# Optimization experiments

Hardware: AMD Instinct MI355X
Metric: run time of the kernel (lower is better)

The kernel has to match this reference:

```python
import jax, jax.numpy as jnp
import numpy as np
from jax import lax

B, C, H, W = 16, 3, 256, 256
K = 3          # lbp kernel size (odd)
POOL = 3       # avg pool size (odd so shapes are preserved)
Q = 8          # quant_len


def _build_lbp_kernel():
    mid = K // 2
    idx_pairs = [((0, 0), (K - 1, K - 1)), ((0, mid), (K - 1, mid)),
                 ((0, K - 1), (K - 1, 0)), ((mid, K - 1), (mid, 0))]
    ks = []
    for a, b in idx_pairs:
        for pos in (a, b):
            k = np.zeros((C, K, K), np.float32)
            k[:, mid, mid] = 1.0
            k[:, pos[0], pos[1]] = -1.0
            ks.append(k)
    return jnp.asarray(np.stack(ks))  # [8, C, K, K]

LBP_KERNEL = _build_lbp_kernel()
# cartesian_prod(arange(Q), arange(Q)) -> first coord slowest (row-major)
IDXS = jnp.asarray(np.stack(np.meshgrid(np.arange(Q), np.arange(Q), indexing='ij'), -1)
                   .reshape(Q * Q, 2).astype(np.float32))  # [64, 2]


def _forward(x, w_expand, b_expand, w_conv, b_conv, w_final, b_final, clamp_low, clamp_high):
    b = x.shape[0]
    # avg_pool2d(kernel=POOL, stride=1, pad=POOL//2, count_include_pad=True)
    p = POOL // 2
    xp = jnp.pad(x, ((0, 0), (0, 0), (p, p), (p, p)))
    x = lax.reduce_window(xp, 0.0, lax.add, (1, 1, POOL, POOL), (1, 1, 1, 1), 'VALID') / (POOL * POOL)
    # 8-channel LBP difference conv, 'same' padding
    x = lax.conv_general_dilated(x, LBP_KERNEL, (1, 1), ((K // 2, K // 2), (K // 2, K // 2)),
                                 dimension_numbers=('NCHW', 'OIHW', 'NCHW'))  # [B,8,H,W]
    x = jnp.clip(x, clamp_low[0], clamp_high[0])
    b4 = b * 4
    v = x.reshape(b4, 2, H * W)                    # pairwise channels
    mn = v.min(-1)                                 # [b4,2]
    mx = v.max(-1)
    lev = mn[..., None] + (mx - mn)[..., None] * (jnp.arange(Q, dtype=v.dtype) / Q)  # [b4,2,Q]
    hi = jnp.concatenate([lev[..., 1:], mx[..., None]], -1)                          # [b4,2,Q]
    vq = v[:, :, None, :]                                                            # [b4,2,1,HW]
    # keep value if lev[l] <= v <= hi[l], else 0 (values equal to a boundary land in both bins)
    masked = jnp.where((vq >= lev[..., None]) & (vq <= hi[..., None]), vq, 0.0)      # [b4,2,Q,HW]
    # joint weighted histogram: sum_p v0[p in bin i] * v1[p in bin j]
    hist = jnp.einsum('bip,bjp->bij', masked[:, 0], masked[:, 1])                    # [b4,Q,Q]
    hist = (hist / jnp.sum(hist)).reshape(b4, Q * Q)
    feats = jnp.concatenate([jnp.broadcast_to(IDXS, (b4, Q * Q, 2)), hist[..., None]], -1)  # [b4,64,3]
    f = feats.reshape(b, 4, Q * Q, 3).transpose(0, 3, 1, 2)                          # [B,3,4,64]
    y = jax.nn.leaky_relu(jnp.einsum('bchw,oc->bohw', f, w_expand) + b_expand[None, :, None, None])
    y = y.transpose(0, 2, 3, 1)                                                      # [B,4,64,56]
    # torch nearest interpolate: src = floor(dst * in / out)
    h_in, w_in = y.shape[-2], y.shape[-1]
    rows = (jnp.arange(H) * h_in) // H
    cols = (jnp.arange(W) * w_in) // W
    y = y[:, :, rows][:, :, :, cols]                                                 # [B,4,H,W]
    # layer_norm over last two dims, no affine
    mean = y.mean((-2, -1), keepdims=True)
    var = ((y - mean) ** 2).mean((-2, -1), keepdims=True)
    y = (y - mean) / jnp.sqrt(var + 1e-5)
    y = jax.nn.leaky_relu(jnp.einsum('bchw,oc->bohw', y, w_conv) + b_conv[None, :, None, None])
    y = lax.conv_general_dilated(y, w_final, (1, 1), ((1, 1), (1, 1)),
                                 dimension_numbers=('NCHW', 'OIHW', 'NCHW')) + b_final[None, :, None, None]
    return jax.nn.leaky_relu(y)                                                      # [B,1,H,W]


def setup_inputs() -> dict:
    key = jax.random.key(0)
    ks = jax.random.split(key, 7)
    return {
        'x': jax.random.normal(ks[0], (B, C, H, W), jnp.float32),
        'w_expand': jax.random.normal(ks[1], (56, 3), jnp.float32) * 0.1,
        'b_expand': jax.random.normal(ks[2], (56,), jnp.float32) * 0.1,
        'w_conv': jax.random.normal(ks[3], (16, 4), jnp.float32) * 0.1,
        'b_conv': jax.random.normal(ks[4], (16,), jnp.float32) * 0.1,
        'w_final': jax.random.normal(ks[5], (1, 16, 3, 3), jnp.float32) * 0.1,
        'b_final': jax.random.normal(ks[6], (1,), jnp.float32) * 0.1,
        'clamp_low': jnp.full((1,), -150.0, jnp.float32),
        'clamp_high': jnp.full((1,), 150.0, jnp.float32),
    }


def reference(x, w_expand, b_expand, w_conv, b_conv, w_final, b_final, clamp_low, clamp_high):
    return _forward(x, w_expand, b_expand, w_conv, b_conv, w_final, b_final, clamp_low, clamp_high)
```

## Files before the change

### kernel.cpp

```cpp
#include <hip/hip_runtime.h>
#include <math.h>

#define NB   16
#define HW   65536
#define NCHH 16

#define OFF_S    0
#define OFF_D    0
#define OFF_PH   1048576
#define OFF_PMN  1114112
#define OFF_PMX  1122304
#define OFF_PT   1130496

__device__ __forceinline__ float leakyf(float v) { return v >= 0.f ? v : 0.01f * v; }

__global__ void __launch_bounds__(256) k_boxmm(const float* __restrict__ x,
                                               const float* __restrict__ clo,
                                               const float* __restrict__ chi,
                                               float* __restrict__ ws)
{
    __shared__ float inp[36][37];
    __shared__ float S[34][36];
    const int doy[8] = {-1, 1, -1, 1, -1, 1, 0, 0};
    const int dox[8] = {-1, 1,  0, 0,  1, -1, 1, -1};
    int b = blockIdx.z;
    int h0 = blockIdx.y * 32, w0 = blockIdx.x * 32;
    int tid = threadIdx.x;
    const float* xb = x + (size_t)b * 3 * HW;
    for (int i = tid; i < 36 * 36; i += 256) {
        int lh = i / 36, lw = i % 36;
        int gh = h0 - 2 + lh, gw = w0 - 2 + lw;
        float v = 0.f;
        if ((unsigned)gh < 256u && (unsigned)gw < 256u) {
            int p = gh * 256 + gw;
            v = xb[p] + xb[HW + p] + xb[2 * HW + p];
        }
        inp[lh][lw] = v;
    }
    __syncthreads();
    for (int i = tid; i < 34 * 34; i += 256) {
        int lh = i / 34, lw = i % 34;
        float s = 0.f;
        #pragma unroll
        for (int dy = 0; dy < 3; ++dy)
            #pragma unroll
            for (int dx = 0; dx < 3; ++dx)
                s += inp[lh + dy][lw + dx];
        S[lh][lw] = s / 9.0f;
    }
    __syncthreads();
    #pragma unroll
    for (int i = 0; i < 4; ++i) {
        int idx = i * 256 + tid;
        int r = idx >> 5, c = idx & 31;
        ws[OFF_S + b * HW + (h0 + r) * 256 + (w0 + c)] = S[r + 1][c + 1];
    }
    float lo = clo[0], hi = chi[0];
    float vmn[8], vmx[8];
    #pragma unroll
    for (int o = 0; o < 8; ++o) { vmn[o] = 3.4e38f; vmx[o] = -3.4e38f; }
    #pragma unroll
    for (int i = 0; i < 4; ++i) {
        int idx = i * 256 + tid;
        int r = idx >> 5, c = idx & 31;
        int gh = h0 + r, gw = w0 + c;
        float sc = S[r + 1][c + 1];
        #pragma unroll
        for (int o = 0; o < 8; ++o) {
            int nh = gh + doy[o], nw = gw + dox[o];
            float off = ((unsigned)nh < 256u && (unsigned)nw < 256u)
                        ? S[r + 1 + doy[o]][c + 1 + dox[o]] : 0.f;
            float v = fminf(fmaxf(sc - off, lo), hi);
            vmn[o] = fminf(vmn[o], v);
            vmx[o] = fmaxf(vmx[o], v);
        }
    }
    #pragma unroll
    for (int o = 0; o < 8; ++o) {
        #pragma unroll
        for (int m = 1; m < 64; m <<= 1) {
            vmn[o] = fminf(vmn[o], __shfl_xor(vmn[o], m));
            vmx[o] = fmaxf(vmx[o], __shfl_xor(vmx[o], m));
        }
    }
    __shared__ float smn[4][8], smx[4][8];
    int wid = tid >> 6, lane = tid & 63;
    if (lane == 0) {
        #pragma unroll
        for (int o = 0; o < 8; ++o) { smn[wid][o] = vmn[o]; smx[wid][o] = vmx[o]; }
    }
    __syncthreads();
    if (tid < 8) {
        int o = tid;
        int tile = blockIdx.y * 8 + blockIdx.x;
        float mn = fminf(fminf(smn[0][o], smn[1][o]), fminf(smn[2][o], smn[3][o]));
        float mx = fmaxf(fmaxf(smx[0][o], smx[1][o]), fmaxf(smx[2][o], smx[3][o]));
        ws[OFF_PMN + (b * 8 + o) * 64 + tile] = mn;
        ws[OFF_PMX + (b * 8 + o) * 64 + tile] = mx;
    }
}

__global__ void __launch_bounds__(256) k_hist_part(const float* __restrict__ clo,
                                                   const float* __restrict__ chi,
                                                   float* ws)
{
    __shared__ float lh[64 * 64];
    __shared__ float sred[4];
    const int doy[8] = {-1, 1, -1, 1, -1, 1, 0, 0};
    const int dox[8] = {-1, 1,  0, 0,  1, -1, 1, -1};
    int bg = blockIdx.x / NCHH;
    int ch = blockIdx.x % NCHH;
    int b = bg >> 2, g = bg & 3;
    int dy0 = doy[2 * g], dx0 = dox[2 * g];
    int dy1 = doy[2 * g + 1], dx1 = dox[2 * g + 1];
    int tid = threadIdx.x;
    int warp = tid >> 6, lane = tid & 63;
    {
        int c0 = (b * 8 + 2 * g) * 64, c1 = (b * 8 + 2 * g + 1) * 64;
        float v;
        if      (warp == 0) v = ws[OFF_PMN + c0 + lane];
        else if (warp == 1) v = ws[OFF_PMX + c0 + lane];
        else if (warp == 2) v = ws[OFF_PMN + c1 + lane];
        else                v = ws[OFF_PMX + c1 + lane];
        bool isMin = (warp & 1) == 0;
        #pragma unroll
        for (int m = 1; m < 64; m <<= 1) {
            float o = __shfl_xor(v, m);
            v = isMin ? fminf(v, o) : fmaxf(v, o);
        }
        if (lane == 0) sred[warp] = v;
    }
    for (int i = tid; i < 4096; i += 256) lh[i] = 0.f;
    __syncthreads();
    float mn0 = sred[0], mx0 = sred[1], mn1 = sred[2], mx1 = sred[3];
    float r0 = mx0 - mn0, r1 = mx1 - mn1;
    float lev0[8], lev1[8];
    #pragma unroll
    for (int q = 0; q < 8; ++q) {
        lev0[q] = __fadd_rn(mn0, __fmul_rn(r0, (float)q * 0.125f));
        lev1[q] = __fadd_rn(mn1, __fmul_rn(r1, (float)q * 0.125f));
    }
    const float* Sb = ws + OFF_S + b * HW;
    int col = tid & 63;
    float lo = clo[0], hi = chi[0];
    int base = ch * (HW / NCHH);
    #pragma unroll
    for (int it = 0; it < (HW / NCHH) / 256; ++it) {
        int p = base + it * 256 + tid;
        int h = p >> 8, w = p & 255;
        float off0 = 0.f, off1 = 0.f;
        int nh = h + dy0, nw = w + dx0;
        if ((unsigned)nh < 256u && (unsigned)nw < 256u) off0 = Sb[nh * 256 + nw];
        nh = h + dy1; nw = w + dx1;
        if ((unsigned)nh < 256u && (unsigned)nw < 256u) off1 = Sb[nh * 256 + nw];
        float sc = Sb[p];
        float v0 = fminf(fmaxf(sc - off0, lo), hi);
        float v1 = fminf(fmaxf(sc - off1, lo), hi);
        int i0 = 0, j0 = 0;
        bool ilo = false, jlo = false;
        #pragma unroll
        for (int k = 1; k < 8; ++k) {
            i0 += (v0 >= lev0[k]); ilo |= (v0 == lev0[k]);
            j0 += (v1 >= lev1[k]); jlo |= (v1 == lev1[k]);
        }
        float prod = v0 * v1;
        atomicAdd(&lh[(i0 * 8 + j0) * 64 + col], prod);
        if (ilo)        atomicAdd(&lh[((i0 - 1) * 8 + j0) * 64 + col], prod);
        if (jlo)        atomicAdd(&lh[(i0 * 8 + (j0 - 1)) * 64 + col], prod);
        if (ilo && jlo) atomicAdd(&lh[((i0 - 1) * 8 + (j0 - 1)) * 64 + col], prod);
    }
    __syncthreads();
    if (tid < 64) {
        int bin = tid;
        float s = 0.f;
        for (int c = 0; c < 64; ++c) s += lh[bin * 64 + ((c + bin) & 63)];
        ws[OFF_PH + blockIdx.x * 64 + bin] = s;
        float t = s;
        #pragma unroll
        for (int m = 1; m < 64; m <<= 1) t += __shfl_xor(t, m);
        if (bin == 0) ws[OFF_PT + blockIdx.x] = t;
    }
}

__global__ void __launch_bounds__(256) k_fuse(const float* __restrict__ we,
                                              const float* __restrict__ be,
                                              const float* __restrict__ wc,
                                              const float* __restrict__ bc,
                                              const float* __restrict__ wf,
                                              float* ws)
{
    __shared__ float sh_hist[256];
    __shared__ float sh_red[256];
    __shared__ float sh_wf[144];
    __shared__ float sh_we[168];
    __shared__ float sh_be[56];
    __shared__ float sh_wc[64];
    __shared__ float sh_bc[16];
    __shared__ float sh_stat[8];
    __shared__ float sw[4][8];
    __shared__ float sh_tot;
    int b     = blockIdx.x / 7;
    int slice = blockIdx.x % 7;
    int tid = threadIdx.x;

    {
        int g = tid >> 6, bin = tid & 63;
        float s = 0.f;
        #pragma unroll
        for (int c = 0; c < NCHH; ++c)
            s += ws[OFF_PH + ((b * 4 + g) * NCHH + c) * 64 + bin];
        sh_hist[tid] = s;
    }
    {
        float s = ws[OFF_PT + tid] + ws[OFF_PT + 256 + tid]
                + ws[OFF_PT + 512 + tid] + ws[OFF_PT + 768 + tid];
        sh_red[tid] = s;
    }
    if (tid < 144) sh_wf[tid] = wf[tid];
    if (tid < 168) sh_we[tid] = we[tid];
    if (tid < 56)  sh_be[tid] = be[tid];
    if (tid < 64)  sh_wc[tid] = wc[tid];
    if (tid < 16)  sh_bc[tid] = bc[tid];
    __syncthreads();
    for (int k = 128; k > 0; k >>= 1) {
        if (tid < k) sh_red[tid] += sh_red[tid + k];
        __syncthreads();
    }
    if (tid == 0) sh_tot = sh_red[0];
    __syncthreads();
    float total = sh_tot;

    float ls[4] = {0.f, 0.f, 0.f, 0.f}, lss[4] = {0.f, 0.f, 0.f, 0.f};
    for (int it = 0; it < 14; ++it) {
        int rem = it * 256 + tid;
        int q = rem / 56, o = rem % 56;
        float base = sh_we[o * 3 + 0] * (float)(q >> 3)
                   + sh_we[o * 3 + 1] * (float)(q & 7) + sh_be[o];
        float w2 = sh_we[o * 3 + 2];
        int cnt = ((32 * (o + 1) + 6) / 7) - ((32 * o + 6) / 7);
        float wgt = (float)(4 * cnt);
        #pragma unroll
        for (int g = 0; g < 4; ++g) {
            float y = leakyf(base + w2 * (sh_hist[g * 64 + q] / total));
            ls[g]  += y * wgt;
            lss[g] += y * y * wgt;
        }
    }
    #pragma unroll
    for (int g = 0; g < 4; ++g) {
        #pragma unroll
        for (int m = 1; m < 64; m <<= 1) {
            ls[g]  += __shfl_xor(ls[g], m);
            lss[g] += __shfl_xor(lss[g], m);
        }
    }
    int wid = tid >> 6, lane = tid & 63;
    if (lane == 0) {
        #pragma unroll
        for (int g = 0; g < 4; ++g) { sw[wid][g] = ls[g]; sw[wid][4 + g] = lss[g]; }
    }
    __syncthreads();
    if (tid < 4) {
        float m  = (sw[0][tid] + sw[1][tid] + sw[2][tid] + sw[3][tid]) / 65536.f;
        float sq = (sw[0][4 + tid] + sw[1][4 + tid] + sw[2][4 + tid] + sw[3][4 + tid]) / 65536.f;
        sh_stat[tid] = m;
        sh_stat[4 + tid] = 1.f / sqrtf(sq - m * m + 1e-5f);
    }
    __syncthreads();

    for (int it = slice * 2; it < slice * 2 + 2; ++it) {
        int rem = it * 256 + tid;
        int q = rem / 56, o = rem % 56;
        float base = sh_we[o * 3 + 0] * (float)(q >> 3)
                   + sh_we[o * 3 + 1] * (float)(q & 7) + sh_be[o];
        float w2 = sh_we[o * 3 + 2];
        float yn[4];
        #pragma unroll
        for (int g = 0; g < 4; ++g) {
            float y = leakyf(base + w2 * (sh_hist[g * 64 + q] / total));
            yn[g] = (y - sh_stat[g]) * sh_stat[4 + g];
        }
        float d[9] = {0.f, 0.f, 0.f, 0.f, 0.f, 0.f, 0.f, 0.f, 0.f};
        #pragma unroll
        for (int c = 0; c < 16; ++c) {
            float z = sh_bc[c];
            #pragma unroll
            for (int g = 0; g < 4; ++g) z += sh_wc[c * 4 + g] * yn[g];
            z = leakyf(z);
            #pragma unroll
            for (int t = 0; t < 9; ++t) d[t] += z * sh_wf[c * 9 + t];
        }
        #pragma unroll
        for (int t = 0; t < 9; ++t)
            ws[OFF_D + (b * 9 + t) * 3584 + rem] = d[t];
    }
}

__global__ void __launch_bounds__(256) k_final(const float* __restrict__ ws,
                                               const float* __restrict__ bf,
                                               float* __restrict__ out)
{
    int t4 = blockIdx.x * 256 + threadIdx.x;
    int b = t4 >> 14;
    int rem = t4 & 16383;
    int h = rem >> 6, w0 = (rem & 63) * 4;
    const float* Db = ws + OFF_D + b * 9 * 3584;
    float bias = bf[0];
    float acc[4] = {bias, bias, bias, bias};
    #pragma unroll
    for (int kh = 0; kh < 3; ++kh) {
        int h2 = h + kh - 1;
        if ((unsigned)h2 > 255u) continue;
        int qr = h2 >> 2;
        #pragma unroll
        for (int kw = 0; kw < 3; ++kw) {
            const float* Dt = Db + (kh * 3 + kw) * 3584 + qr * 56;
            #pragma unroll
            for (int j = 0; j < 4; ++j) {
                int w2 = w0 + j + kw - 1;
                if ((unsigned)w2 <= 255u) acc[j] += Dt[(w2 * 7) >> 5];
            }
        }
    }
    float4 o4;
    o4.x = leakyf(acc[0]); o4.y = leakyf(acc[1]);
    o4.z = leakyf(acc[2]); o4.w = leakyf(acc[3]);
    ((float4*)out)[t4] = o4;
}

extern "C" void kernel_launch(void* const* d_in, const int* in_sizes, int n_in,
                              void* d_out, int out_size, void* d_ws, size_t ws_size,
                              hipStream_t stream)
{
    const float* x   = (const float*)d_in[0];
    const float* we  = (const float*)d_in[1];
    const float* be  = (const float*)d_in[2];
    const float* wc  = (const float*)d_in[3];
    const float* bc  = (const float*)d_in[4];
    const float* wf  = (const float*)d_in[5];
    const float* bfi = (const float*)d_in[6];
    const float* clo = (const float*)d_in[7];
    const float* chi = (const float*)d_in[8];
    float* out = (float*)d_out;
    float* ws  = (float*)d_ws;

    k_boxmm<<<dim3(8, 8, NB), 256, 0, stream>>>(x, clo, chi, ws);
    k_hist_part<<<64 * NCHH, 256, 0, stream>>>(clo, chi, ws);
    k_fuse<<<NB * 7, 256, 0, stream>>>(we, be, wc, bc, wf, ws);
    k_final<<<1024, 256, 0, stream>>>(ws, bfi, out);
}
```

Baseline: 131.5 us.

## Fuse histogram-feature and final conv kernels into one kernel with shared-memory D tile

Merges k_fuse and k_final into a single kernel. Each of 1024 blocks recomputes the per-batch statistics, then computes only the three quantized rows of the D table it needs into shared memory and applies the final 3x3 conv directly. This removes one kernel launch and the global round trip for the D intermediate. In exchange, every block redundantly repeats the histogram reduction and the mean/variance pass, which was previously spread over only 112 blocks. It also flattens k_boxmm's grid to 1D and vectorises the shared-memory zeroing in k_hist_part, both minor.

```diff
diff --git a/kernel.cpp b/kernel.cpp
--- a/kernel.cpp
+++ b/kernel.cpp
@@ -6,7 +6,6 @@
 #define NCHH 16
 
 #define OFF_S    0
-#define OFF_D    0
 #define OFF_PH   1048576
 #define OFF_PMN  1114112
 #define OFF_PMX  1122304
@@ -21,11 +20,13 @@
 {
     __shared__ float inp[36][37];
     __shared__ float S[34][36];
+    __shared__ float smn[4][8], smx[4][8];
     const int doy[8] = {-1, 1, -1, 1, -1, 1, 0, 0};
     const int dox[8] = {-1, 1,  0, 0,  1, -1, 1, -1};
-    int b = blockIdx.z;
-    int h0 = blockIdx.y * 32, w0 = blockIdx.x * 32;
+    int b = blockIdx.x >> 6, tile = blockIdx.x & 63;
+    int h0 = (tile >> 3) * 32, w0 = (tile & 7) * 32;
     int tid = threadIdx.x;
+    float lo = clo[0], hi = chi[0];
     const float* xb = x + (size_t)b * 3 * HW;
     for (int i = tid; i < 36 * 36; i += 256) {
         int lh = i / 36, lw = i % 36;
@@ -55,7 +56,6 @@
         int r = idx >> 5, c = idx & 31;
         ws[OFF_S + b * HW + (h0 + r) * 256 + (w0 + c)] = S[r + 1][c + 1];
     }
-    float lo = clo[0], hi = chi[0];
     float vmn[8], vmx[8];
     #pragma unroll
     for (int o = 0; o < 8; ++o) { vmn[o] = 3.4e38f; vmx[o] = -3.4e38f; }
@@ -83,7 +83,6 @@
             vmx[o] = fmaxf(vmx[o], __shfl_xor(vmx[o], m));
         }
     }
-    __shared__ float smn[4][8], smx[4][8];
     int wid = tid >> 6, lane = tid & 63;
     if (lane == 0) {
         #pragma unroll
@@ -92,7 +91,6 @@
     __syncthreads();
     if (tid < 8) {
         int o = tid;
-        int tile = blockIdx.y * 8 + blockIdx.x;
         float mn = fminf(fminf(smn[0][o], smn[1][o]), fminf(smn[2][o], smn[3][o]));
         float mx = fmaxf(fmaxf(smx[0][o], smx[1][o]), fmaxf(smx[2][o], smx[3][o]));
         ws[OFF_PMN + (b * 8 + o) * 64 + tile] = mn;
@@ -108,8 +106,7 @@
     __shared__ float sred[4];
     const int doy[8] = {-1, 1, -1, 1, -1, 1, 0, 0};
     const int dox[8] = {-1, 1,  0, 0,  1, -1, 1, -1};
-    int bg = blockIdx.x / NCHH;
-    int ch = blockIdx.x % NCHH;
+    int bg = blockIdx.x >> 4, ch = blockIdx.x & 15;
     int b = bg >> 2, g = bg & 3;
     int dy0 = doy[2 * g], dx0 = dox[2 * g];
     int dy1 = doy[2 * g + 1], dx1 = dox[2 * g + 1];
@@ -130,7 +127,11 @@
         }
         if (lane == 0) sred[warp] = v;
     }
-    for (int i = tid; i < 4096; i += 256) lh[i] = 0.f;
+    {
+        float4 z4 = {0.f, 0.f, 0.f, 0.f};
+        float4* l4 = (float4*)lh;
+        l4[tid] = z4; l4[tid + 256] = z4; l4[tid + 512] = z4; l4[tid + 768] = z4;
+    }
     __syncthreads();
     float mn0 = sred[0], mx0 = sred[1], mn1 = sred[2], mx1 = sred[3];
     float r0 = mx0 - mn0, r1 = mx1 - mn1;
@@ -182,12 +183,14 @@
     }
 }
 
-__global__ void __launch_bounds__(256) k_fuse(const float* __restrict__ we,
-                                              const float* __restrict__ be,
-                                              const float* __restrict__ wc,
-                                              const float* __restrict__ bc,
-                                              const float* __restrict__ wf,
-                                              float* ws)
+__global__ void __launch_bounds__(256) k_fuse_final(const float* __restrict__ we,
+                                                    const float* __restrict__ be,
+                                                    const float* __restrict__ wc,
+                                                    const float* __restrict__ bc,
+                                                    const float* __restrict__ wf,
+                                                    const float* __restrict__ bf,
+                                                    const float* __restrict__ ws,
+                                                    float* __restrict__ out)
 {
     __shared__ float sh_hist[256];
     __shared__ float sh_red[256];
@@ -199,9 +202,11 @@
     __shared__ float sh_stat[8];
     __shared__ float sw[4][8];
     __shared__ float sh_tot;
-    int b     = blockIdx.x / 7;
-    int slice = blockIdx.x % 7;
+    __shared__ float Dl[9][3][56];
+    int bid = blockIdx.x;
     int tid = threadIdx.x;
+    int b = bid >> 6, k = bid & 63;
+    int qr_base = k - 1;
 
     {
         int g = tid >> 6, bin = tid & 63;
@@ -211,19 +216,16 @@
             s += ws[OFF_PH + ((b * 4 + g) * NCHH + c) * 64 + bin];
         sh_hist[tid] = s;
     }
-    {
-        float s = ws[OFF_PT + tid] + ws[OFF_PT + 256 + tid]
+    sh_red[tid] = ws[OFF_PT + tid] + ws[OFF_PT + 256 + tid]
                 + ws[OFF_PT + 512 + tid] + ws[OFF_PT + 768 + tid];
-        sh_red[tid] = s;
-    }
     if (tid < 144) sh_wf[tid] = wf[tid];
     if (tid < 168) sh_we[tid] = we[tid];
     if (tid < 56)  sh_be[tid] = be[tid];
     if (tid < 64)  sh_wc[tid] = wc[tid];
     if (tid < 16)  sh_bc[tid] = bc[tid];
     __syncthreads();
-    for (int k = 128; k > 0; k >>= 1) {
-        if (tid < k) sh_red[tid] += sh_red[tid + k];
+    for (int s = 128; s > 0; s >>= 1) {
+        if (tid < s) sh_red[tid] += sh_red[tid + s];
         __syncthreads();
     }
     if (tid == 0) sh_tot = sh_red[0];
@@ -234,14 +236,14 @@
     for (int it = 0; it < 14; ++it) {
         int rem = it * 256 + tid;
         int q = rem / 56, o = rem % 56;
-        float base = sh_we[o * 3 + 0] * (float)(q >> 3)
-                   + sh_we[o * 3 + 1] * (float)(q & 7) + sh_be[o];
+        float basev = sh_we[o * 3 + 0] * (float)(q >> 3)
+                    + sh_we[o * 3 + 1] * (float)(q & 7) + sh_be[o];
         float w2 = sh_we[o * 3 + 2];
         int cnt = ((32 * (o + 1) + 6) / 7) - ((32 * o + 6) / 7);
         float wgt = (float)(4 * cnt);
         #pragma unroll
         for (int g = 0; g < 4; ++g) {
-            float y = leakyf(base + w2 * (sh_hist[g * 64 + q] / total));
+            float y = leakyf(basev + w2 * (sh_hist[g * 64 + q] / total));
             ls[g]  += y * wgt;
             lss[g] += y * y * wgt;
         }
@@ -262,70 +264,68 @@
     __syncthreads();
     if (tid < 4) {
         float m  = (sw[0][tid] + sw[1][tid] + sw[2][tid] + sw[3][tid]) / 65536.f;
-        float sq = (sw[0][4 + tid] + sw[1][4 + tid] + sw[2][4 + tid] + sw[3][4 + tid]) / 65536.f;
+        float sq = (sw[0][4 + tid] + sw[1][4 + tid]
+                  + sw[2][4 + tid] + sw[3][4 + tid]) / 65536.f;
         sh_stat[tid] = m;
         sh_stat[4 + tid] = 1.f / sqrtf(sq - m * m + 1e-5f);
     }
     __syncthreads();
 
-    for (int it = slice * 2; it < slice * 2 + 2; ++it) {
-        int rem = it * 256 + tid;
-        int q = rem / 56, o = rem % 56;
-        float base = sh_we[o * 3 + 0] * (float)(q >> 3)
-                   + sh_we[o * 3 + 1] * (float)(q & 7) + sh_be[o];
-        float w2 = sh_we[o * 3 + 2];
-        float yn[4];
-        #pragma unroll
-        for (int g = 0; g < 4; ++g) {
-            float y = leakyf(base + w2 * (sh_hist[g * 64 + q] / total));
-            yn[g] = (y - sh_stat[g]) * sh_stat[4 + g];
-        }
-        float d[9] = {0.f, 0.f, 0.f, 0.f, 0.f, 0.f, 0.f, 0.f, 0.f};
-        #pragma unroll
-        for (int c = 0; c < 16; ++c) {
-            float z = sh_bc[c];
-            #pragma unroll
-            for (int g = 0; g < 4; ++g) z += sh_wc[c * 4 + g] * yn[g];
-            z = leakyf(z);
-            #pragma unroll
-            for (int t = 0; t < 9; ++t) d[t] += z * sh_wf[c * 9 + t];
-        }
-        #pragma unroll
-        for (int t = 0; t < 9; ++t)
-            ws[OFF_D + (b * 9 + t) * 3584 + rem] = d[t];
-    }
-}
-
-__global__ void __launch_bounds__(256) k_final(const float* __restrict__ ws,
-                                               const float* __restrict__ bf,
-                                               float* __restrict__ out)
-{
-    int t4 = blockIdx.x * 256 + threadIdx.x;
-    int b = t4 >> 14;
-    int rem = t4 & 16383;
-    int h = rem >> 6, w0 = (rem & 63) * 4;
-    const float* Db = ws + OFF_D + b * 9 * 3584;
-    float bias = bf[0];
-    float acc[4] = {bias, bias, bias, bias};
-    #pragma unroll
-    for (int kh = 0; kh < 3; ++kh) {
-        int h2 = h + kh - 1;
-        if ((unsigned)h2 > 255u) continue;
-        int qr = h2 >> 2;
-        #pragma unroll
-        for (int kw = 0; kw < 3; ++kw) {
-            const float* Dt = Db + (kh * 3 + kw) * 3584 + qr * 56;
-            #pragma unroll
-            for (int j = 0; j < 4; ++j) {
-                int w2 = w0 + j + kw - 1;
-                if ((unsigned)w2 <= 255u) acc[j] += Dt[(w2 * 7) >> 5];
+    if (tid < 168) {
+        int i = tid / 56, o = tid % 56;
+        int q = qr_base + i;
+        if ((unsigned)q < 64u) {
+            float basev = sh_we[o * 3 + 0] * (float)(q >> 3)
+                        + sh_we[o * 3 + 1] * (float)(q & 7) + sh_be[o];
+            float w2 = sh_we[o * 3 + 2];
+            float yn[4];
+            #pragma unroll
+            for (int g = 0; g < 4; ++g) {
+                float y = leakyf(basev + w2 * (sh_hist[g * 64 + q] / total));
+                yn[g] = (y - sh_stat[g]) * sh_stat[4 + g];
             }
-        }
-    }
-    float4 o4;
-    o4.x = leakyf(acc[0]); o4.y = leakyf(acc[1]);
-    o4.z = leakyf(acc[2]); o4.w = leakyf(acc[3]);
-    ((float4*)out)[t4] = o4;
+            float d[9] = {0.f, 0.f, 0.f, 0.f, 0.f, 0.f, 0.f, 0.f, 0.f};
+            #pragma unroll
+            for (int c = 0; c < 16; ++c) {
+                float z = sh_bc[c];
+                #pragma unroll
+                for (int g = 0; g < 4; ++g) z += sh_wc[c * 4 + g] * yn[g];
+                z = leakyf(z);
+                #pragma unroll
+                for (int t = 0; t < 9; ++t) d[t] += z * sh_wf[c * 9 + t];
+            }
+            #pragma unroll
+            for (int t = 0; t < 9; ++t) Dl[t][i][o] = d[t];
+        }
+    }
+    __syncthreads();
+
+    {
+        int t4 = bid * 256 + tid;
+        int rem = t4 & 16383;
+        int h = rem >> 6, w0 = (rem & 63) * 4;
+        float bias = bf[0];
+        float acc[4] = {bias, bias, bias, bias};
+        #pragma unroll
+        for (int kh = 0; kh < 3; ++kh) {
+            int h2 = h + kh - 1;
+            if ((unsigned)h2 > 255u) continue;
+            int i = (h2 >> 2) - qr_base;
+            #pragma unroll
+            for (int kw = 0; kw < 3; ++kw) {
+                const float* Dt = &Dl[kh * 3 + kw][i][0];
+                #pragma unroll
+                for (int j = 0; j < 4; ++j) {
+                    int w2 = w0 + j + kw - 1;
+                    if ((unsigned)w2 <= 255u) acc[j] += Dt[(w2 * 7) >> 5];
+                }
+            }
+        }
+        float4 o4;
+        o4.x = leakyf(acc[0]); o4.y = leakyf(acc[1]);
+        o4.z = leakyf(acc[2]); o4.w = leakyf(acc[3]);
+        ((float4*)out)[t4] = o4;
+    }
 }
 
 extern "C" void kernel_launch(void* const* d_in, const int* in_sizes, int n_in,
@@ -344,8 +344,7 @@
     float* out = (float*)d_out;
     float* ws  = (float*)d_ws;
 
-    k_boxmm<<<dim3(8, 8, NB), 256, 0, stream>>>(x, clo, chi, ws);
-    k_hist_part<<<64 * NCHH, 256, 0, stream>>>(clo, chi, ws);
-    k_fuse<<<NB * 7, 256, 0, stream>>>(we, be, wc, bc, wf, ws);
-    k_final<<<1024, 256, 0, stream>>>(ws, bfi, out);
+    k_boxmm<<<1024, 256, 0, stream>>>(x, clo, chi, ws);
+    k_hist_part<<<1024, 256, 0, stream>>>(clo, chi, ws);
+    k_fuse_final<<<1024, 256, 0, stream>>>(we, be, wc, bc, wf, bfi, ws, out);
 }
```

Result: no change. 133.0 us (+1.1%).
